# Performance work log

Hardware: AMD Instinct MI355X
Metric: run time of the kernel (lower is better)

Reference implementation:

```python
import jax, jax.numpy as jnp
import numpy as np

N = 50000      # nodes
E = 600000     # edges
IN = 128       # in_channels
C = 32         # hidden_channels
H = 4          # heads
L = 3          # num_layers
NEG_SLOPE = 0.2


def setup_inputs() -> dict:
    key = jax.random.key(0)
    ks = jax.random.split(key, 2 + 6 * L)
    d = {
        "x": jax.random.normal(ks[0], (N, IN), jnp.float32),
        "edge_index": jax.random.randint(ks[1], (2, E), 0, N, dtype=jnp.int64),
    }
    dims_in = [IN, H * C, H * C]
    s = 0.1
    for l in range(L):
        kk = ks[2 + 6 * l: 2 + 6 * (l + 1)]
        out_dim = H * C if l < L - 1 else C
        d[f"W{l}"] = jax.random.normal(kk[0], (dims_in[l], H * C), jnp.float32) * s
        d[f"linb{l}"] = jnp.zeros((H * C,), jnp.float32)
        d[f"att{l}"] = jax.random.normal(kk[1], (H, C), jnp.float32) * s
        d[f"bias{l}"] = jnp.zeros((out_dim,), jnp.float32)
        d[f"skipW{l}"] = jax.random.normal(kk[2], (dims_in[l], out_dim), jnp.float32) * s
        d[f"skipb{l}"] = jnp.zeros((out_dim,), jnp.float32)
    return d


def _gatv2_layer(x, src, dst, W, linb, att, bias, concat):
    # share_weights=True and x_target == x  ->  single projection for src & dst
    n = x.shape[0]
    h = (x @ W + linb).reshape(n, H, C)                      # [N,H,C]
    e = jax.nn.leaky_relu(h[src] + h[dst], NEG_SLOPE)        # [E,H,C]
    score = jnp.einsum('ehc,hc->eh', e, att)                 # [E,H]
    # scatter-softmax over incoming edges of each destination node
    m = jax.ops.segment_max(score, dst, num_segments=n)      # [N,H]
    p = jnp.exp(score - m[dst])                              # [E,H]
    denom = jax.ops.segment_sum(p, dst, num_segments=n)      # [N,H]
    alpha = p / jnp.maximum(denom[dst], 1e-16)               # [E,H]
    out = jax.ops.segment_sum(alpha[:, :, None] * h[src], dst, num_segments=n)  # [N,H,C]
    out = out.reshape(n, H * C) if concat else out.mean(axis=1)
    return out + bias


def reference(x, edge_index,
              W0, linb0, att0, bias0, skipW0, skipb0,
              W1, linb1, att1, bias1, skipW1, skipb1,
              W2, linb2, att2, bias2, skipW2, skipb2):
    src, dst = edge_index[0], edge_index[1]
    params = [
        (W0, linb0, att0, bias0, skipW0, skipb0),
        (W1, linb1, att1, bias1, skipW1, skipb1),
        (W2, linb2, att2, bias2, skipW2, skipb2),
    ]
    for l, (W, linb, att, bias, sW, sb) in enumerate(params):
        out = _gatv2_layer(x, src, dst, W, linb, att, bias, concat=(l < L - 1))
        x = out + (x @ sW + sb)                              # skip connection
        if l != L - 1:
            x = jax.nn.elu(x)                                # dropout is identity in eval mode
    return x
```

## Files before the change

kernel.cpp:

```cpp
#include <hip/hip_runtime.h>
#include <hip/hip_bf16.h>

#define NN 50000
#define NE 600000
#define IN_DIM 128
#define HC 128
#define NH 4
#define NC 32
#define NEG_SLOPE 0.2f

#define NTHR 256
#define NTILE 196
#define WT_TOTAL 86016
#define NG32 1563
#define GHIST 2344
#define NGAT16 3125

typedef __attribute__((ext_vector_type(8))) short short8;
typedef __attribute__((ext_vector_type(4))) float floatx4;
typedef __attribute__((ext_vector_type(8))) unsigned short ushort8v;

__device__ __forceinline__ float bf2f(unsigned short u) {
    return __uint_as_float(((unsigned)u) << 16);
}
__device__ __forceinline__ unsigned short f2bf(float f) {
    unsigned u = __float_as_uint(f);
    unsigned r = (u + 0x7FFFu + ((u >> 16) & 1u)) >> 16;
    return (unsigned short)r;
}

template<int OD, int NTC, int PITX, int PITO>
__device__ __forceinline__ void gemm16_lds(
    const unsigned short (* __restrict__ xt)[PITX], const unsigned short* __restrict__ Wt,
    const float* __restrict__ b, unsigned short (* __restrict__ tile)[PITO],
    int c016, int lane) {
    int quad = lane >> 4, l16 = lane & 15;
    floatx4 acc[NTC];
    #pragma unroll
    for (int j = 0; j < NTC; ++j) acc[j] = (floatx4){0.f, 0.f, 0.f, 0.f};
    int lidx = (quad * 16 + l16) * 8;

    #pragma unroll
    for (int ks = 0; ks < 4; ++ks) {
        int kb = ks * 32 + quad * 8;
        short8 xb = *(const short8*)&xt[l16][kb];
        #pragma unroll
        for (int tc = 0; tc < NTC; ++tc) {
            int grp = ks * (OD / 16) + c016 + tc;
            short8 af = *(const short8*)&Wt[grp * 512 + lidx];
            acc[tc] = __builtin_amdgcn_mfma_f32_16x16x32_bf16(af, xb, acc[tc], 0, 0, 0);
        }
    }

    #pragma unroll
    for (int tc = 0; tc < NTC; ++tc) {
        int cbase = (c016 + tc) * 16 + quad * 4;
        float4 bv = *(const float4*)&b[cbase];
        ushort4 pk = {f2bf(acc[tc][0] + bv.x), f2bf(acc[tc][1] + bv.y),
                      f2bf(acc[tc][2] + bv.z), f2bf(acc[tc][3] + bv.w)};
        *(ushort4*)&tile[l16][cbase] = pk;
    }
}

__device__ __forceinline__ void store_tile128(
    const unsigned short (* __restrict__ tile)[136],
    unsigned short* __restrict__ y, int n0, int pt) {
    #pragma unroll
    for (int s = 0; s < 4; ++s) {
        int idx = s * 128 + pt;
        int node = idx >> 4, t16 = idx & 15;
        if (n0 + node < NN)
            *(ushort8v*)&y[(size_t)(n0 + node) * 128 + t16 * 8] =
                *(const ushort8v*)&tile[node][t16 * 8];
    }
}

template<int SOD>
__global__ __launch_bounds__(256) void k_gat_gemm(
    const unsigned short* __restrict__ h, const int* __restrict__ rowptr,
    const int* __restrict__ csr_src, const float* __restrict__ att,
    const float* __restrict__ gbias, const unsigned short* __restrict__ gskip,
    const unsigned short* __restrict__ WtA, const float* __restrict__ linb,
    unsigned short* __restrict__ yh,
    const unsigned short* __restrict__ WtB, const float* __restrict__ skipb,
    unsigned short* __restrict__ yskip) {
    __shared__ unsigned short xt[16][136];
    __shared__ unsigned short th[16][136];
    __shared__ unsigned short ts[16][136];

    int lane = threadIdx.x & 63;
    int wid = threadIdx.x >> 6;
    int slot = lane >> 4, t = lane & 15;
    int lbase = slot << 4;
    int nloc = wid * 4 + slot;
    int nv = blockIdx.x * 16 + nloc;
    bool valid = nv < NN;
    int n = valid ? nv : NN - 1;

    ushort8v skv = *(const ushort8v*)(gskip + (size_t)n * HC + t * 8);

    int beg = rowptr[n], end = rowptr[n + 1];
    int deg = end - beg;
    int idv = 0;
    if (t < deg) idv = csr_src[beg + t];

    ushort8v hdv = *(const ushort8v*)(h + (size_t)n * HC + t * 8);
    float hd[8], av[8];
    #pragma unroll
    for (int c = 0; c < 8; ++c) hd[c] = bf2f(hdv[c]);
    float4 av0 = ((const float4*)att)[t * 2];
    float4 av1 = ((const float4*)att)[t * 2 + 1];
    av[0] = av0.x; av[1] = av0.y; av[2] = av0.z; av[3] = av0.w;
    av[4] = av1.x; av[5] = av1.y; av[6] = av1.z; av[7] = av1.w;

    float K = 0.f;
    #pragma unroll
    for (int c = 0; c < 8; ++c) K = fmaf(hd[c], av[c], K);

    const unsigned short* hp = h + t * 8;
    int id0 = __shfl(idv, lbase + 0, 64);
    int id1 = __shfl(idv, lbase + 1, 64);
    int id2 = __shfl(idv, lbase + 2, 64);
    int id3 = __shfl(idv, lbase + 3, 64);
    ushort8v g0 = 0, g1 = 0, g2 = 0, g3 = 0;
    if (deg > 0) g0 = *(const ushort8v*)(hp + id0);
    if (deg > 1) g1 = *(const ushort8v*)(hp + id1);
    if (deg > 2) g2 = *(const ushort8v*)(hp + id2);
    if (deg > 3) g3 = *(const ushort8v*)(hp + id3);

    float l = 0.f;
    float acc[8] = {};

    auto gstep = [&](ushort8v& G, int k) {
        float hs[8];
        float S1 = K, S2 = 0.f;
        #pragma unroll
        for (int c = 0; c < 8; ++c) {
            float hsv = bf2f(G[c]);
            hs[c] = hsv;
            S1 = fmaf(hsv, av[c], S1);
            S2 = fmaf(fabsf(hsv + hd[c]), av[c], S2);
        }
        int kn = k + 4;
        if (kn < deg) {
            int idn = (kn < 16) ? __shfl(idv, lbase + kn, 64) : csr_src[beg + kn];
            G = *(const ushort8v*)(hp + idn);
        }
        float part = fmaf(0.6f, S1, 0.4f * S2);
        part += __shfl_xor(part, 1, 64);
        part += __shfl_xor(part, 2, 64);
        float p = __expf(part);
        #pragma unroll
        for (int c = 0; c < 8; ++c) acc[c] = fmaf(p, hs[c], acc[c]);
        l += p;
    };

    int k = 0;
    if (deg > 0) for (;;) {
        gstep(g0, k); if (++k >= deg) break;
        gstep(g1, k); if (++k >= deg) break;
        gstep(g2, k); if (++k >= deg) break;
        gstep(g3, k); if (++k >= deg) break;
    }

    float inv = 1.f / fmaxf(l, 1e-16f);
    float4 bv0 = ((const float4*)gbias)[t * 2];
    float4 bv1 = ((const float4*)gbias)[t * 2 + 1];
    float bb[8] = {bv0.x, bv0.y, bv0.z, bv0.w, bv1.x, bv1.y, bv1.z, bv1.w};
    ushort8v ov;
    #pragma unroll
    for (int c = 0; c < 8; ++c) {
        float r = acc[c] * inv + bb[c] + bf2f(skv[c]);
        r = r > 0.f ? r : (__expf(r) - 1.f);
        ov[c] = f2bf(r);
    }
    *(ushort8v*)&xt[nloc][t * 8] = ov;

    __syncthreads();

    if (wid < 2)           gemm16_lds<128, 4, 136, 136>(xt, WtA, linb, th, wid * 4, lane);
    else if (SOD == 128)   gemm16_lds<128, 4, 136, 136>(xt, WtB, skipb, ts, (wid - 2) * 4, lane);
    else                   gemm16_lds<32, 1, 136, 136>(xt, WtB, skipb, ts, wid - 2, lane);

    __syncthreads();

    int p = threadIdx.x;
    {
        int node = p >> 4, t16 = p & 15;
        int gn = blockIdx.x * 16 + node;
        if (gn < NN)
            *(ushort8v*)&yh[(size_t)gn * 128 + t16 * 8] = *(const ushort8v*)&th[node][t16 * 8];
    }
    if (SOD == 128) {
        int node = p >> 4, t16 = p & 15;
        int gn = blockIdx.x * 16 + node;
        if (gn < NN)
            *(ushort8v*)&yskip[(size_t)gn * 128 + t16 * 8] = *(const ushort8v*)&ts[node][t16 * 8];
    } else {
        if (p < 64) {
            int node = p >> 2, t4 = p & 3;
            int gn = blockIdx.x * 16 + node;
            if (gn < NN)
                *(ushort8v*)&yskip[(size_t)gn * 32 + t4 * 8] = *(const ushort8v*)&ts[node][t4 * 8];
        }
    }
}

__global__ __launch_bounds__(256) void k_gat_last(
    const unsigned short* __restrict__ h, const int* __restrict__ rowptr,
    const int* __restrict__ csr_src, const float* __restrict__ att,
    const float* __restrict__ bias, const unsigned short* __restrict__ skip,
    float* __restrict__ out) {
    int lane = threadIdx.x & 63;
    int wid = threadIdx.x >> 6;
    int slot = lane >> 4, t = lane & 15;
    int lbase = slot << 4;

    int nv = blockIdx.x * 16 + wid * 4 + slot;
    bool valid = nv < NN;
    int n = valid ? nv : NN - 1;

    ushort8v skv = 0;
    if (t < 4) skv = *(const ushort8v*)(skip + (size_t)n * NC + t * 8);

    int beg = rowptr[n], end = rowptr[n + 1];
    int deg = end - beg;
    int idv = 0;
    if (t < deg) idv = csr_src[beg + t];

    ushort8v hdv = *(const ushort8v*)(h + (size_t)n * HC + t * 8);
    float hd[8], av[8];
    #pragma unroll
    for (int c = 0; c < 8; ++c) hd[c] = bf2f(hdv[c]);
    float4 av0 = ((const float4*)att)[t * 2];
    float4 av1 = ((const float4*)att)[t * 2 + 1];
    av[0] = av0.x; av[1] = av0.y; av[2] = av0.z; av[3] = av0.w;
    av[4] = av1.x; av[5] = av1.y; av[6] = av1.z; av[7] = av1.w;

    float K = 0.f;
    #pragma unroll
    for (int c = 0; c < 8; ++c) K = fmaf(hd[c], av[c], K);

    const unsigned short* hp = h + t * 8;
    int id0 = __shfl(idv, lbase + 0, 64);
    int id1 = __shfl(idv, lbase + 1, 64);
    int id2 = __shfl(idv, lbase + 2, 64);
    int id3 = __shfl(idv, lbase + 3, 64);
    ushort8v g0 = 0, g1 = 0, g2 = 0, g3 = 0;
    if (deg > 0) g0 = *(const ushort8v*)(hp + id0);
    if (deg > 1) g1 = *(const ushort8v*)(hp + id1);
    if (deg > 2) g2 = *(const ushort8v*)(hp + id2);
    if (deg > 3) g3 = *(const ushort8v*)(hp + id3);

    float l = 0.f;
    float acc[8] = {};

    auto gstep = [&](ushort8v& G, int k) {
        float hs[8];
        float S1 = K, S2 = 0.f;
        #pragma unroll
        for (int c = 0; c < 8; ++c) {
            float hsv = bf2f(G[c]);
            hs[c] = hsv;
            S1 = fmaf(hsv, av[c], S1);
            S2 = fmaf(fabsf(hsv + hd[c]), av[c], S2);
        }
        int kn = k + 4;
        if (kn < deg) {
            int idn = (kn < 16) ? __shfl(idv, lbase + kn, 64) : csr_src[beg + kn];
            G = *(const ushort8v*)(hp + idn);
        }
        float part = fmaf(0.6f, S1, 0.4f * S2);
        part += __shfl_xor(part, 1, 64);
        part += __shfl_xor(part, 2, 64);
        float p = __expf(part);
        #pragma unroll
        for (int c = 0; c < 8; ++c) acc[c] = fmaf(p, hs[c], acc[c]);
        l += p;
    };

    int k = 0;
    if (deg > 0) for (;;) {
        gstep(g0, k); if (++k >= deg) break;
        gstep(g1, k); if (++k >= deg) break;
        gstep(g2, k); if (++k >= deg) break;
        gstep(g3, k); if (++k >= deg) break;
    }

    float inv = 1.f / fmaxf(l, 1e-16f);
    float o[8];
    #pragma unroll
    for (int c = 0; c < 8; ++c) o[c] = acc[c] * inv;

    float r4[8], r8[8], r12[8];
    #pragma unroll
    for (int c = 0; c < 8; ++c) {
        r4[c]  = __shfl_down(o[c], 4, 16);
        r8[c]  = __shfl_down(o[c], 8, 16);
        r12[c] = __shfl_down(o[c], 12, 16);
    }
    if (t < 4 && valid) {
        float* op = out + (size_t)n * NC + t * 8;
        float rr[8];
        #pragma unroll
        for (int c = 0; c < 8; ++c) {
            rr[c] = 0.25f * (o[c] + r4[c] + r8[c] + r12[c])
                  + bias[t * 8 + c] + bf2f(skv[c]);
        }
        *(float4*)op = (float4){rr[0], rr[1], rr[2], rr[3]};
        *(float4*)(op + 4) = (float4){rr[4], rr[5], rr[6], rr[7]};
    }
}


__global__ void k_prep(const float* __restrict__ W0, const float* __restrict__ S0,
                       const float* __restrict__ W1, const float* __restrict__ S1,
                       const float* __restrict__ W2, const float* __restrict__ S2,
                       unsigned short* __restrict__ wt, int* __restrict__ deg) {
    int idx = blockIdx.x * blockDim.x + threadIdx.x;
    if (idx < WT_TOTAL) {
        if (idx < 81920) {
            int r = idx >> 14;
            const float* W = (r == 0) ? W0 : (r == 1) ? S0 : (r == 2) ? W1 : (r == 3) ? S1 : W2;
            int off = idx & 16383;
            int j = off & 7, l16 = (off >> 3) & 15, quad = (off >> 7) & 3;
            int cg = (off >> 9) & 7, ks = off >> 12;
            int k = ks * 32 + quad * 8 + j;
            int col = cg * 16 + l16;
            wt[idx] = f2bf(W[(size_t)k * 128 + col]);
        } else {
            int off = idx - 81920;
            int j = off & 7, l16 = (off >> 3) & 15, quad = (off >> 7) & 3;
            int cg = (off >> 9) & 1, ks = off >> 10;
            int k = ks * 32 + quad * 8 + j;
            int col = cg * 16 + l16;
            wt[idx] = f2bf(S2[(size_t)k * 32 + col]);
        }
        return;
    }
    int i = idx - WT_TOTAL;
    if (i < NN) deg[i] = 0;
}

__global__ __launch_bounds__(256) void k_gemm0_hist(
    const float* __restrict__ x,
    const unsigned short* __restrict__ Wta, const float* __restrict__ ba, unsigned short* __restrict__ ya,
    const unsigned short* __restrict__ Wtb, const float* __restrict__ bb, unsigned short* __restrict__ yb,
    const int* __restrict__ dst, int* __restrict__ deg) {
    __shared__ unsigned short xt[32][136];
    __shared__ unsigned short tA[32][136];
    __shared__ unsigned short tB[32][136];
    int b = blockIdx.x;
    if (b < NG32) {
        int n0 = b * 32;
        #pragma unroll
        for (int s = 0; s < 4; ++s) {
            int i = s * 256 + threadIdx.x;
            int row = i >> 5, c4 = i & 31;
            int rr = (n0 + row < NN) ? n0 + row : NN - 1;
            float4 v = *(const float4*)&x[(size_t)rr * IN_DIM + c4 * 4];
            ushort4 pk = {f2bf(v.x), f2bf(v.y), f2bf(v.z), f2bf(v.w)};
            *(ushort4*)&xt[row][c4 * 4] = pk;
        }
        __syncthreads();
        int wid = threadIdx.x >> 6, lane = threadIdx.x & 63;
        if (wid < 2) {
            gemm16_lds<128, 4, 136, 136>(xt, Wta, ba, tA, wid * 4, lane);
            gemm16_lds<128, 4, 136, 136>(xt + 16, Wta, ba, tA + 16, wid * 4, lane);
        } else {
            gemm16_lds<128, 4, 136, 136>(xt, Wtb, bb, tB, (wid - 2) * 4, lane);
            gemm16_lds<128, 4, 136, 136>(xt + 16, Wtb, bb, tB + 16, (wid - 2) * 4, lane);
        }
        __syncthreads();
        int pt = threadIdx.x & 127;
        if (threadIdx.x < 128) store_tile128(tA, ya, n0, pt);
        else                   store_tile128(tB, yb, n0, pt);
    } else {
        int e = (b - NG32) * 256 + threadIdx.x;
        if (e < NE) atomicAdd(&deg[dst[e]], 1);
    }
}

__global__ __launch_bounds__(NTHR) void k_scan1(const int* __restrict__ deg,
                                                int* __restrict__ partial,
                                                int* __restrict__ blocksum) {
    __shared__ int sh[NTHR];
    int b = blockIdx.x, t = threadIdx.x;
    int i = b * NTHR + t;
    int d = (i < NN) ? deg[i] : 0;
    sh[t] = d;
    __syncthreads();
    #pragma unroll
    for (int off = 1; off < NTHR; off <<= 1) {
        int v = (t >= off) ? sh[t - off] : 0;
        __syncthreads();
        sh[t] += v;
        __syncthreads();
    }
    if (i < NN) partial[i] = sh[t];
    if (t == NTHR - 1) blocksum[b] = sh[t];
}

__global__ __launch_bounds__(NTHR) void k_scan23(const int* __restrict__ deg,
                                                 const int* __restrict__ partial,
                                                 const int* __restrict__ blocksum,
                                                 int* __restrict__ rowptr,
                                                 int* __restrict__ cursor) {
    __shared__ int sh[NTHR];
    int b = blockIdx.x, t = threadIdx.x;
    int v = (t < NTILE) ? blocksum[t] : 0;
    sh[t] = v;
    __syncthreads();
    #pragma unroll
    for (int off = 1; off < NTHR; off <<= 1) {
        int u = (t >= off) ? sh[t - off] : 0;
        __syncthreads();
        sh[t] += u;
        __syncthreads();
    }
    int tile_off = (b > 0) ? sh[b - 1] : 0;
    int i = b * NTHR + t;
    if (i < NN) {
        int inc = partial[i] + tile_off;
        rowptr[i + 1] = inc;
        cursor[i] = inc - deg[i];
        if (i == 0) rowptr[0] = 0;
    }
}

__global__ void k_scatter(const int* __restrict__ src, const int* __restrict__ dst,
                          int* __restrict__ cursor, int* __restrict__ csr_src) {
    int e = blockIdx.x * blockDim.x + threadIdx.x;
    if (e >= NE) return;
    int d = dst[e];
    int pos = atomicAdd(&cursor[d], 1);
    csr_src[pos] = src[e] * HC;
}

extern "C" void kernel_launch(void* const* d_in, const int* in_sizes, int n_in,
                              void* d_out, int out_size, void* d_ws, size_t ws_size,
                              hipStream_t stream) {
    const float* x0 = (const float*)d_in[0];
    const int* ei = (const int*)d_in[1];
    const int* src = ei;
    const int* dst = ei + NE;

    unsigned short* H0 = (unsigned short*)d_ws;
    unsigned short* S0 = H0 + (size_t)NN * HC;
    unsigned short* H1 = S0 + (size_t)NN * HC;
    unsigned short* S1 = H1 + (size_t)NN * HC;
    int* deg     = (int*)(S1 + (size_t)NN * HC);
    int* rowptr  = deg + NN;
    int* cursor  = rowptr + NN + 1;
    int* partial = cursor + NN;
    int* blocksum = partial + NN;
    uintptr_t pa = (uintptr_t)(blocksum + NTILE);
    pa = (pa + 15) & ~(uintptr_t)15;
    unsigned short* wt = (unsigned short*)pa;
    int* csr_src = (int*)(wt + WT_TOTAL);

    unsigned short* wtW[3] = {wt, wt + 32768, wt + 65536};
    unsigned short* wtS[3] = {wt + 16384, wt + 49152, wt + 81920};

    k_prep<<<(WT_TOTAL + NN + 255) / 256, 256, 0, stream>>>(
        (const float*)d_in[2], (const float*)d_in[6],
        (const float*)d_in[8], (const float*)d_in[12],
        (const float*)d_in[14], (const float*)d_in[18], wt, deg);

    k_gemm0_hist<<<NG32 + GHIST, 256, 0, stream>>>(
        x0, wtW[0], (const float*)d_in[3], H0,
        wtS[0], (const float*)d_in[7], S0, dst, deg);

    k_scan1<<<NTILE, NTHR, 0, stream>>>(deg, partial, blocksum);
    k_scan23<<<NTILE, NTHR, 0, stream>>>(deg, partial, blocksum, rowptr, cursor);
    k_scatter<<<GHIST, 256, 0, stream>>>(src, dst, cursor, csr_src);

    k_gat_gemm<128><<<NGAT16, 256, 0, stream>>>(
        H0, rowptr, csr_src,
        (const float*)d_in[4], (const float*)d_in[5], S0,
        wtW[1], (const float*)d_in[9], H1,
        wtS[1], (const float*)d_in[13], S1);

    k_gat_gemm<32><<<NGAT16, 256, 0, stream>>>(
        H1, rowptr, csr_src,
        (const float*)d_in[10], (const float*)d_in[11], S1,
        wtW[2], (const float*)d_in[15], H0,
        wtS[2], (const float*)d_in[19], S0);

    k_gat_last<<<NGAT16, 256, 0, stream>>>(
        H0, rowptr, csr_src,
        (const float*)d_in[16], (const float*)d_in[17], S0, (float*)d_out);
}
```

Measured before the change: 280.8 us.

## Group nodes by in-degree via counting-sort permutation to balance GAT blocks

Builds a degree histogram (33 bins, descending degree) during the scan and a node permutation during the scatter kernel. The GAT kernels then process nodes in permuted order so each 16-node block and each wavefront handles nodes of similar degree, which reduces divergence and load imbalance in the per-edge loops. The cost is extra atomics on a tiny bin array, an indirection through perm, and scattered (non-contiguous) output and skip/h reads and writes that lose locality.

```diff
diff --git a/kernel.cpp b/kernel.cpp
--- a/kernel.cpp
+++ b/kernel.cpp
@@ -15,6 +15,7 @@
 #define NG32 1563
 #define GHIST 2344
 #define NGAT16 3125
+#define NBIN 33
 
 typedef __attribute__((ext_vector_type(8))) short short8;
 typedef __attribute__((ext_vector_type(4))) float floatx4;
@@ -78,7 +79,8 @@
 template<int SOD>
 __global__ __launch_bounds__(256) void k_gat_gemm(
     const unsigned short* __restrict__ h, const int* __restrict__ rowptr,
-    const int* __restrict__ csr_src, const float* __restrict__ att,
+    const int* __restrict__ csr_src, const int* __restrict__ perm,
+    const float* __restrict__ att,
     const float* __restrict__ gbias, const unsigned short* __restrict__ gskip,
     const unsigned short* __restrict__ WtA, const float* __restrict__ linb,
     unsigned short* __restrict__ yh,
@@ -87,15 +89,17 @@
     __shared__ unsigned short xt[16][136];
     __shared__ unsigned short th[16][136];
     __shared__ unsigned short ts[16][136];
+    __shared__ int pn[16];
 
     int lane = threadIdx.x & 63;
     int wid = threadIdx.x >> 6;
     int slot = lane >> 4, t = lane & 15;
     int lbase = slot << 4;
     int nloc = wid * 4 + slot;
-    int nv = blockIdx.x * 16 + nloc;
-    bool valid = nv < NN;
-    int n = valid ? nv : NN - 1;
+    int nlin = blockIdx.x * 16 + nloc;
+    bool valid = nlin < NN;
+    int n = perm[valid ? nlin : NN - 1];
+    if (t == 0) pn[nloc] = n;
 
     ushort8v skv = *(const ushort8v*)(gskip + (size_t)n * HC + t * 8);
 
@@ -187,28 +191,32 @@
     int p = threadIdx.x;
     {
         int node = p >> 4, t16 = p & 15;
-        int gn = blockIdx.x * 16 + node;
-        if (gn < NN)
+        if (blockIdx.x * 16 + node < NN) {
+            int gn = pn[node];
             *(ushort8v*)&yh[(size_t)gn * 128 + t16 * 8] = *(const ushort8v*)&th[node][t16 * 8];
+        }
     }
     if (SOD == 128) {
         int node = p >> 4, t16 = p & 15;
-        int gn = blockIdx.x * 16 + node;
-        if (gn < NN)
+        if (blockIdx.x * 16 + node < NN) {
+            int gn = pn[node];
             *(ushort8v*)&yskip[(size_t)gn * 128 + t16 * 8] = *(const ushort8v*)&ts[node][t16 * 8];
+        }
     } else {
         if (p < 64) {
             int node = p >> 2, t4 = p & 3;
-            int gn = blockIdx.x * 16 + node;
-            if (gn < NN)
+            if (blockIdx.x * 16 + node < NN) {
+                int gn = pn[node];
                 *(ushort8v*)&yskip[(size_t)gn * 32 + t4 * 8] = *(const ushort8v*)&ts[node][t4 * 8];
+            }
         }
     }
 }
 
 __global__ __launch_bounds__(256) void k_gat_last(
     const unsigned short* __restrict__ h, const int* __restrict__ rowptr,
-    const int* __restrict__ csr_src, const float* __restrict__ att,
+    const int* __restrict__ csr_src, const int* __restrict__ perm,
+    const float* __restrict__ att,
     const float* __restrict__ bias, const unsigned short* __restrict__ skip,
     float* __restrict__ out) {
     int lane = threadIdx.x & 63;
@@ -216,9 +224,9 @@
     int slot = lane >> 4, t = lane & 15;
     int lbase = slot << 4;
 
-    int nv = blockIdx.x * 16 + wid * 4 + slot;
-    bool valid = nv < NN;
-    int n = valid ? nv : NN - 1;
+    int nlin = blockIdx.x * 16 + wid * 4 + slot;
+    bool valid = nlin < NN;
+    int n = perm[valid ? nlin : NN - 1];
 
     ushort8v skv = 0;
     if (t < 4) skv = *(const ushort8v*)(skip + (size_t)n * NC + t * 8);
@@ -316,7 +324,8 @@
 __global__ void k_prep(const float* __restrict__ W0, const float* __restrict__ S0,
                        const float* __restrict__ W1, const float* __restrict__ S1,
                        const float* __restrict__ W2, const float* __restrict__ S2,
-                       unsigned short* __restrict__ wt, int* __restrict__ deg) {
+                       unsigned short* __restrict__ wt, int* __restrict__ deg,
+                       int* __restrict__ bins) {
     int idx = blockIdx.x * blockDim.x + threadIdx.x;
     if (idx < WT_TOTAL) {
         if (idx < 81920) {
@@ -339,7 +348,9 @@
         return;
     }
     int i = idx - WT_TOTAL;
-    if (i < NN) deg[i] = 0;
+    if (i < NN) { deg[i] = 0; return; }
+    int j = i - NN;
+    if (j < NBIN) bins[j] = 0;
 }
 
 __global__ __launch_bounds__(256) void k_gemm0_hist(
@@ -383,11 +394,16 @@
 
 __global__ __launch_bounds__(NTHR) void k_scan1(const int* __restrict__ deg,
                                                 int* __restrict__ partial,
-                                                int* __restrict__ blocksum) {
+                                                int* __restrict__ blocksum,
+                                                int* __restrict__ bins) {
     __shared__ int sh[NTHR];
     int b = blockIdx.x, t = threadIdx.x;
     int i = b * NTHR + t;
     int d = (i < NN) ? deg[i] : 0;
+    if (i < NN) {
+        int bi = 32 - (d > 32 ? 32 : d);
+        atomicAdd(&bins[bi], 1);
+    }
     sh[t] = d;
     __syncthreads();
     #pragma unroll
@@ -405,9 +421,15 @@
                                                  const int* __restrict__ partial,
                                                  const int* __restrict__ blocksum,
                                                  int* __restrict__ rowptr,
-                                                 int* __restrict__ cursor) {
+                                                 int* __restrict__ cursor,
+                                                 const int* __restrict__ bins,
+                                                 int* __restrict__ bincur) {
     __shared__ int sh[NTHR];
     int b = blockIdx.x, t = threadIdx.x;
+    if (b == 0 && t == 0) {
+        int s = 0;
+        for (int q = 0; q < NBIN; ++q) { int c = bins[q]; bincur[q] = s; s += c; }
+    }
     int v = (t < NTILE) ? blocksum[t] : 0;
     sh[t] = v;
     __syncthreads();
@@ -429,12 +451,24 @@
 }
 
 __global__ void k_scatter(const int* __restrict__ src, const int* __restrict__ dst,
-                          int* __restrict__ cursor, int* __restrict__ csr_src) {
-    int e = blockIdx.x * blockDim.x + threadIdx.x;
-    if (e >= NE) return;
-    int d = dst[e];
-    int pos = atomicAdd(&cursor[d], 1);
-    csr_src[pos] = src[e] * HC;
+                          int* __restrict__ cursor, int* __restrict__ csr_src,
+                          const int* __restrict__ deg, int* __restrict__ bincur,
+                          int* __restrict__ perm) {
+    int b = blockIdx.x;
+    if (b < GHIST) {
+        int e = b * 256 + threadIdx.x;
+        if (e >= NE) return;
+        int d = dst[e];
+        int pos = atomicAdd(&cursor[d], 1);
+        csr_src[pos] = src[e] * HC;
+    } else {
+        int i = (b - GHIST) * 256 + threadIdx.x;
+        if (i >= NN) return;
+        int d = deg[i];
+        int bi = 32 - (d > 32 ? 32 : d);
+        int pos = atomicAdd(&bincur[bi], 1);
+        perm[pos] = i;
+    }
 }
 
 extern "C" void kernel_launch(void* const* d_in, const int* in_sizes, int n_in,
@@ -454,7 +488,10 @@
     int* cursor  = rowptr + NN + 1;
     int* partial = cursor + NN;
     int* blocksum = partial + NN;
-    uintptr_t pa = (uintptr_t)(blocksum + NTILE);
+    int* bins    = blocksum + NTILE;
+    int* bincur  = bins + NBIN;
+    int* perm    = bincur + NBIN;
+    uintptr_t pa = (uintptr_t)(perm + NN);
     pa = (pa + 15) & ~(uintptr_t)15;
     unsigned short* wt = (unsigned short*)pa;
     int* csr_src = (int*)(wt + WT_TOTAL);
@@ -462,32 +499,32 @@
     unsigned short* wtW[3] = {wt, wt + 32768, wt + 65536};
     unsigned short* wtS[3] = {wt + 16384, wt + 49152, wt + 81920};
 
-    k_prep<<<(WT_TOTAL + NN + 255) / 256, 256, 0, stream>>>(
+    k_prep<<<(WT_TOTAL + NN + NBIN + 255) / 256, 256, 0, stream>>>(
         (const float*)d_in[2], (const float*)d_in[6],
         (const float*)d_in[8], (const float*)d_in[12],
-        (const float*)d_in[14], (const float*)d_in[18], wt, deg);
+        (const float*)d_in[14], (const float*)d_in[18], wt, deg, bins);
 
     k_gemm0_hist<<<NG32 + GHIST, 256, 0, stream>>>(
         x0, wtW[0], (const float*)d_in[3], H0,
         wtS[0], (const float*)d_in[7], S0, dst, deg);
 
-    k_scan1<<<NTILE, NTHR, 0, stream>>>(deg, partial, blocksum);
-    k_scan23<<<NTILE, NTHR, 0, stream>>>(deg, partial, blocksum, rowptr, cursor);
-    k_scatter<<<GHIST, 256, 0, stream>>>(src, dst, cursor, csr_src);
+    k_scan1<<<NTILE, NTHR, 0, stream>>>(deg, partial, blocksum, bins);
+    k_scan23<<<NTILE, NTHR, 0, stream>>>(deg, partial, blocksum, rowptr, cursor, bins, bincur);
+    k_scatter<<<GHIST + NTILE, 256, 0, stream>>>(src, dst, cursor, csr_src, deg, bincur, perm);
 
     k_gat_gemm<128><<<NGAT16, 256, 0, stream>>>(
-        H0, rowptr, csr_src,
+        H0, rowptr, csr_src, perm,
         (const float*)d_in[4], (const float*)d_in[5], S0,
         wtW[1], (const float*)d_in[9], H1,
         wtS[1], (const float*)d_in[13], S1);
 
     k_gat_gemm<32><<<NGAT16, 256, 0, stream>>>(
-        H1, rowptr, csr_src,
+        H1, rowptr, csr_src, perm,
         (const float*)d_in[10], (const float*)d_in[11], S1,
         wtW[2], (const float*)d_in[15], H0,
         wtS[2], (const float*)d_in[19], S0);
 
     k_gat_last<<<NGAT16, 256, 0, stream>>>(
-        H0, rowptr, csr_src,
+        H0, rowptr, csr_src, perm,
         (const float*)d_in[16], (const float*)d_in[17], S0, (float*)d_out);
 }
```

New measurement: 572.2 us. 2.04x slower.
